# Kernel tuning notes

Hardware: AMD Instinct MI355X
Metric: run time of the kernel (lower is better)

## Reference

```python
import jax, jax.numpy as jnp
import numpy as np
from jax import lax

# Lens/aperture geometry (must match init_kwargs lens_mask)
LENS = 21
RADIUS = LENS // 2
EPS = 1e-8


def _offsets():
    """Flattened 21x21 aperture footprint: distance kernel, circular lens mask,
    and (row, col) slice offsets into the padded image."""
    ys, xs = np.meshgrid(np.arange(LENS), np.arange(LENS), indexing='ij')
    dy = ys - RADIUS
    dx = xs - RADIUS
    dist = np.sqrt(dy * dy + dx * dx).astype(np.float32)
    mask = (dist <= RADIUS).astype(np.float32)
    return (jnp.asarray(dist.ravel()), jnp.asarray(mask.ravel()),
            jnp.asarray(ys.ravel().astype(np.int32)),
            jnp.asarray(xs.ravel().astype(np.int32)))


def scatter_layer(x5, lens_effect):
    """Scatter (splat) defocus rendering of one RGBAD layer.

    x5: [B,5,H,W] (r,g,b,alpha,relative-disparity); lens_effect: [B,1].
    Each source pixel splats its premultiplied color over a disk of radius
    r = |disp| * lens_effect (soft-edged, area-normalized). Because the disk
    kernel is symmetric in the offset, the scatter is computed as a gather
    over the 21x21 footprint with weights taken from the *source* pixel.

    Returns [B,5,H,W]: [:3] accumulated rgb, [3] accumulated weight,
    [4] occupancy (clipped accumulated alpha-weight).
    """
    B, _, H, W = x5.shape
    dist, mask, oy, ox = _offsets()
    rgb, a, disp = x5[:, :3], x5[:, 3:4], x5[:, 4:5]
    r = jnp.clip(jnp.abs(disp) * lens_effect[:, :, None, None], 0.0, float(RADIUS))  # [B,1,H,W]

    # per-source-pixel soft disk area: sum_o mask(o) * clip(r + 0.5 - dist(o), 0, 1)
    def area_step(acc, dm):
        d, m = dm
        return acc + m * jnp.clip(r + 0.5 - d, 0.0, 1.0), None

    area, _ = lax.scan(area_step, jnp.zeros_like(r), (dist, mask))

    # premultiplied source energy, normalized by splat area
    s = jnp.concatenate([rgb * a, a], axis=1) / (area + EPS)  # [B,4,H,W]
    pad = ((0, 0), (0, 0), (RADIUS, RADIUS), (RADIUS, RADIUS))
    s_pad = jnp.pad(s, pad)
    r_pad = jnp.pad(r, pad)

    # gather formulation of the scatter: out[q] = sum_o s[q-o] * w(o; r[q-o])
    def step(acc, dmyx):
        d, m, dy, dx = dmyx
        sl = lax.dynamic_slice(s_pad, (0, 0, dy, dx), (B, 4, H, W))
        rsl = lax.dynamic_slice(r_pad, (0, 0, dy, dx), (B, 1, H, W))
        w = m * jnp.clip(rsl + 0.5 - d, 0.0, 1.0)
        return acc + sl * w, None

    out4, _ = lax.scan(step, jnp.zeros((B, 4, H, W), x5.dtype), (dist, mask, oy, ox))
    occu = jnp.clip(out4[:, 3:4], 0.0, 1.0)
    return jnp.concatenate([out4, occu], axis=1)


def setup_inputs() -> dict:
    key = jax.random.key(0)
    k1, k2 = jax.random.split(key)
    B, N_LAYER, H, W = 2, 3, 512, 512
    rgbad_layers = jax.random.uniform(k1, (B, 5 * N_LAYER, H, W), dtype=jnp.float32)
    # lens strength in a range that exercises the full 21x21 footprint
    lens_effect = jax.random.uniform(k2, (B, 1), dtype=jnp.float32) * 10.0
    focal = jnp.zeros((B, 5 * N_LAYER, H, W), dtype=jnp.float32)
    return {"rgbad_layers": rgbad_layers, "lens_effect": lens_effect, "focal": focal}


def reference(rgbad_layers, lens_effect, focal):
    """Multi_Layer_Renderer.forward: front-to-back alpha compositing of
    per-layer scatter-rendered bokeh."""
    x = rgbad_layers - focal
    n_layer = x.shape[1] // 5
    blurs = [scatter_layer(x[:, 5 * i:5 * (i + 1)], lens_effect) for i in range(n_layer)]
    rgb0, w0, o0 = blurs[0][:, :3], blurs[0][:, 3:4], blurs[0][:, 4:5]
    blur_rgb = rgb0 / (w0 + EPS) * o0
    trans = 1.0 - o0  # accumulated transmittance
    for li in range(1, n_layer):
        lr, lw, lo = blurs[li][:, :3], blurs[li][:, 3:4], blurs[li][:, 4:5]
        blur_rgb = blur_rgb + lr / (lw + EPS) * (trans * lo)
        trans = trans * (1.0 - lo)
    return blur_rgb
```

## Files before the change

kernel.cpp:

```cpp
#include <hip/hip_runtime.h>
#include <hip/hip_bf16.h>

#define HH 512
#define WW 512
#define HWSZ (512*512)

typedef _Float16 hh4 __attribute__((ext_vector_type(4)));
typedef _Float16 hh2 __attribute__((ext_vector_type(2)));
typedef float    ff4 __attribute__((ext_vector_type(4)));

__device__ __forceinline__ float clamp01(float x) {
    return __builtin_amdgcn_fmed3f(x, 0.0f, 1.0f);
}
__device__ __forceinline__ hh2 clamp01h2(hh2 x) {
    const hh2 z = {(_Float16)0.0f, (_Float16)0.0f};
    const hh2 o = {(_Float16)1.0f, (_Float16)1.0f};
    return __builtin_elementwise_min(__builtin_elementwise_max(x, z), o);
}
__device__ __forceinline__ hh2 pkrtz(float a, float b) {
    return __builtin_bit_cast(hh2, __builtin_amdgcn_cvt_pkrtz(a, b));
}

__global__ __launch_bounds__(256, 2)
void mlr_fused_kernel(const float* __restrict__ rgbad,
                      const float* __restrict__ lens_eff,
                      const float* __restrict__ focal,
                      float* __restrict__ out,
                      int nbx, int B)
{
    constexpr int TW = 64, TH = 16;
    constexpr int SW = 88;
    constexpr int SH = TH + 20;
    constexpr int LP = 90;
    constexpr int NG = SW / 4;
    constexpr int NSLOT = SH * NG;
    constexpr int NIT = (NSLOT + 255) / 256;

    __shared__ uint2 sP[SH * LP];
    __shared__ uint  rP[SH * LP / 2];
    __shared__ int   maxbits;

    const int tx  = threadIdx.x;
    const int ty  = threadIdx.y;
    const int tid = ty * 16 + tx;
    const int bid = blockIdx.x;
    const int bb  = bid % B;
    const int t   = bid / B;
    const int bx0 = (t % nbx) * TW;
    const int by0 = (t / nbx) * TH;
    const float lens = lens_eff[bb];

    static constexpr float DJ[44] = {
        0.f, 1.f, 1.41421356f, 2.f, 2.23606798f, 2.82842712f, 3.f, 3.16227766f,
        3.60555128f, 4.f, 4.12310563f, 4.24264069f, 4.47213595f, 5.f, 5.09901951f,
        5.38516481f, 5.65685425f, 5.83095189f, 6.f, 6.08276253f, 6.32455532f,
        6.40312424f, 6.70820393f, 7.f, 7.07106781f, 7.21110255f, 7.28010989f,
        7.61577311f, 7.81024968f, 8.f, 8.06225775f, 8.24621125f, 8.48528137f,
        8.54400375f, 8.60232527f, 8.94427191f, 9.f, 9.05538514f, 9.21954446f,
        9.43398113f, 9.48683298f, 9.84885780f, 9.89949494f, 10.f };
    static constexpr float CNT[44] = {
        1,4,4,4,8,4,4,8,8,4,8,4,8,12,8,8,4,8,4,8,8,8,
        8,4,12,8,8,8,8,4,16,8,4,8,8,8,4,8,16,8,8,8,4,12 };

    float blurR[4] = {0,0,0,0}, blurG[4] = {0,0,0,0}, blurB[4] = {0,0,0,0};
    float trans[4] = {1,1,1,1};

#pragma unroll 1
    for (int l = 0; l < 3; ++l) {
        __syncthreads();
        if (tid == 0) maxbits = 0;
        __syncthreads();

        const float* pin = rgbad + (size_t)(bb * 15 + 5 * l) * HWSZ;
        const float* pfo = focal + (size_t)(bb * 15 + 5 * l) * HWSZ;
        float mloc = 0.f;

#pragma unroll
        for (int it = 0; it < NIT; ++it) {
            int s = tid + it * 256;
            s = (s < NSLOT) ? s : (NSLOT - 1);
            const int row = s / NG;
            const int grp = s - row * NG;
            const int gy  = by0 - 10 + row;
            const int gx0 = bx0 - 12 + 4 * grp;

            ff4 i0 = {0,0,0,0}, i1 = {0,0,0,0}, i2 = {0,0,0,0}, i3 = {0,0,0,0}, i4 = {0,0,0,0};
            ff4 f0 = {0,0,0,0}, f1 = {0,0,0,0}, f2 = {0,0,0,0}, f3 = {0,0,0,0}, f4 = {0,0,0,0};
            const bool valid = ((unsigned)gy < (unsigned)HH) && ((unsigned)gx0 < (unsigned)WW);
            if (valid) {
                const size_t off = (size_t)gy * WW + (size_t)gx0;
                i0 = *reinterpret_cast<const ff4*>(pin + off);
                i1 = *reinterpret_cast<const ff4*>(pin + off +   HWSZ);
                i2 = *reinterpret_cast<const ff4*>(pin + off + 2*HWSZ);
                i3 = *reinterpret_cast<const ff4*>(pin + off + 3*HWSZ);
                i4 = *reinterpret_cast<const ff4*>(pin + off + 4*HWSZ);
                f0 = *reinterpret_cast<const ff4*>(pfo + off);
                f1 = *reinterpret_cast<const ff4*>(pfo + off +   HWSZ);
                f2 = *reinterpret_cast<const ff4*>(pfo + off + 2*HWSZ);
                f3 = *reinterpret_cast<const ff4*>(pfo + off + 3*HWSZ);
                f4 = *reinterpret_cast<const ff4*>(pfo + off + 4*HWSZ);
            }
            uint2 pk[4];
            unsigned short rh[4];
#pragma unroll
            for (int k = 0; k < 4; ++k) {
                const float cr = i0[k] - f0[k];
                const float cg = i1[k] - f1[k];
                const float cb = i2[k] - f2[k];
                const float ca = i3[k] - f3[k];
                const float cd = i4[k] - f4[k];
                const float r  = fminf(fabsf(cd) * lens, 10.f);
                const float rp05 = r + 0.5f;
                const hh2 rp2s = pkrtz(rp05, rp05);
                float aacc = 0.f;
#pragma unroll
                for (int j = 0; j < 44; j += 2) {
                    const hh2 dj2 = {(_Float16)DJ[j], (_Float16)DJ[j + 1]};
                    const hh2 c2  = {(_Float16)CNT[j], (_Float16)CNT[j + 1]};
                    const hh2 w2  = clamp01h2(rp2s - dj2);
                    aacc = __builtin_amdgcn_fdot2(w2, c2, aacc, false);
                }
                const float inv = 1.0f / (aacc + 1e-8f);
                const float pa  = ca * inv;
                hh4 hv;
                hv.x = (_Float16)(cr * pa);
                hv.y = (_Float16)(cg * pa);
                hv.z = (_Float16)(cb * pa);
                hv.w = (_Float16)pa;
                pk[k] = __builtin_bit_cast(uint2, hv);
                rh[k] = __builtin_bit_cast(unsigned short, (_Float16)rp05);
                mloc  = fmaxf(mloc, rp05);
            }
            const int base = row * LP + 4 * grp;
            uint4 s01, s23;
            s01.x = pk[0].x; s01.y = pk[0].y; s01.z = pk[1].x; s01.w = pk[1].y;
            s23.x = pk[2].x; s23.y = pk[2].y; s23.z = pk[3].x; s23.w = pk[3].y;
            *reinterpret_cast<uint4*>(&sP[base])     = s01;
            *reinterpret_cast<uint4*>(&sP[base + 2]) = s23;
            uint2 rr2;
            rr2.x = (uint)rh[0] | ((uint)rh[1] << 16);
            rr2.y = (uint)rh[2] | ((uint)rh[3] << 16);
            *reinterpret_cast<uint2*>(&rP[base >> 1]) = rr2;
        }
        atomicMax(&maxbits, __float_as_int(mloc));
        __syncthreads();

        const float rmax = __int_as_float(maxbits);
        const int U = min(10, (int)ceilf(rmax) - 1);

        float accR[4] = {0,0,0,0}, accG[4] = {0,0,0,0};
        float accB[4] = {0,0,0,0}, accW[4] = {0,0,0,0};

#define PAIRD(v0) { \
            const uint4 sp = *reinterpret_cast<const uint4*>(&sP[rbase + (v0)]); \
            const hh2 rp2 = __builtin_bit_cast(hh2, rP[(rbase + (v0)) >> 1]); \
            const hh2 cR = __builtin_bit_cast(hh2, __builtin_amdgcn_perm(sp.z, sp.x, 0x05040100u)); \
            const hh2 cG = __builtin_bit_cast(hh2, __builtin_amdgcn_perm(sp.z, sp.x, 0x07060302u)); \
            const hh2 cB = __builtin_bit_cast(hh2, __builtin_amdgcn_perm(sp.w, sp.y, 0x05040100u)); \
            const hh2 cA = __builtin_bit_cast(hh2, __builtin_amdgcn_perm(sp.w, sp.y, 0x07060302u)); \
            _Pragma("unroll") \
            for (int ox = 0; ox < 4; ++ox) { \
                const hh2 w2 = clamp01h2(rp2 - hdd2[(v0) - ox + 13]); \
                accR[ox] = __builtin_amdgcn_fdot2(cR, w2, accR[ox], false); \
                accG[ox] = __builtin_amdgcn_fdot2(cG, w2, accG[ox], false); \
                accB[ox] = __builtin_amdgcn_fdot2(cB, w2, accB[ox], false); \
                accW[ox] = __builtin_amdgcn_fdot2(cA, w2, accW[ox], false); \
            } }

#pragma unroll 1
        for (int u = -U; u <= U; ++u) {
            const float u2f = (float)(u * u);
            const float vm2 = rmax * rmax - u2f;
            hh2 hdd2[26];
#pragma unroll
            for (int m = 0; m < 26; ++m) {
                const int dxa = m - 13, dxb = dxa + 1;
                const float qa = u2f + (float)(dxa * dxa);
                const float qb = u2f + (float)(dxb * dxb);
                const float da = (qa <= 100.0f) ? __builtin_sqrtf(qa) : 3000.0f;
                const float db = (qb <= 100.0f) ? __builtin_sqrtf(qb) : 3000.0f;
                hdd2[m] = pkrtz(da, db);
            }
            const int rbase = (ty + 10 + u) * LP + 12 + 4 * tx;

            PAIRD(-2) PAIRD(0) PAIRD(2) PAIRD(4)
            if (vm2 > 9.0f)  { PAIRD(-6) PAIRD(-4) PAIRD(6) PAIRD(8) }
            if (vm2 > 36.0f) { PAIRD(-8) PAIRD(10) }
            if (vm2 > 81.0f) { PAIRD(-10) PAIRD(12) }
        }
#undef PAIRD

#pragma unroll
        for (int ox = 0; ox < 4; ++ox) {
            const float wsum = accW[ox];
            const float occ  = clamp01(wsum);
            const float f    = trans[ox] * occ / (wsum + 1e-8f);
            blurR[ox] = fmaf(accR[ox], f, blurR[ox]);
            blurG[ox] = fmaf(accG[ox], f, blurG[ox]);
            blurB[ox] = fmaf(accB[ox], f, blurB[ox]);
            trans[ox] *= (1.0f - occ);
        }
    }

    const int oy = by0 + ty;
    const size_t obase = (size_t)bb * 3 * HWSZ + (size_t)oy * WW + (size_t)(bx0 + 4 * tx);

    float4 vR, vG, vB;
    vR.x = blurR[0]; vR.y = blurR[1]; vR.z = blurR[2]; vR.w = blurR[3];
    vG.x = blurG[0]; vG.y = blurG[1]; vG.z = blurG[2]; vG.w = blurG[3];
    vB.x = blurB[0]; vB.y = blurB[1]; vB.z = blurB[2]; vB.w = blurB[3];

    *reinterpret_cast<float4*>(out + obase)            = vR;
    *reinterpret_cast<float4*>(out + obase + HWSZ)     = vG;
    *reinterpret_cast<float4*>(out + obase + 2 * HWSZ) = vB;
}

extern "C" void kernel_launch(void* const* d_in, const int* in_sizes, int n_in,
                              void* d_out, int out_size, void* d_ws, size_t ws_size,
                              hipStream_t stream) {
    const float* rgbad = (const float*)d_in[0];
    const float* lens  = (const float*)d_in[1];
    const float* focal = (const float*)d_in[2];
    float* out = (float*)d_out;
    const int B = in_sizes[1];
    const int nbx = WW / 64;
    const int nby = HH / 16;
    dim3 grid(nbx * nby * B, 1, 1);
    dim3 block(16, 16, 1);
    hipLaunchKernelGGL(mlr_fused_kernel, grid, block, 0, stream,
                       rgbad, lens, focal, out, nbx, B);
}
```

Before: 43.99 us.

## Compute two output rows per thread and share shared-memory loads across rows

Each thread now computes a 2-row by 4-column output block, using a 32x32 tile and a 128-thread block. Each loaded source row is used for two output rows at vertical offsets u and u-1, with the distance table from the previous iteration carried forward as the second row's table. This roughly halves LDS loads and distance-table builds per output. It costs more registers (doubled accumulators and two 26-entry tables), and the taller halo means more loaded pixels per output tile.

```diff
diff --git a/kernel.cpp b/kernel.cpp
--- a/kernel.cpp
+++ b/kernel.cpp
@@ -8,6 +8,14 @@
 typedef _Float16 hh4 __attribute__((ext_vector_type(4)));
 typedef _Float16 hh2 __attribute__((ext_vector_type(2)));
 typedef float    ff4 __attribute__((ext_vector_type(4)));
+
+constexpr int TW = 32, TH = 32;
+constexpr int SW = 56;
+constexpr int SH = 52;
+constexpr int LP = 60;
+constexpr int NG = SW / 4;
+constexpr int NSLOT = SH * NG;
+constexpr int NIT = 6;
 
 __device__ __forceinline__ float clamp01(float x) {
     return __builtin_amdgcn_fmed3f(x, 0.0f, 1.0f);
@@ -21,28 +29,20 @@
     return __builtin_bit_cast(hh2, __builtin_amdgcn_cvt_pkrtz(a, b));
 }
 
-__global__ __launch_bounds__(256, 2)
+__global__ __launch_bounds__(128, 2)
 void mlr_fused_kernel(const float* __restrict__ rgbad,
                       const float* __restrict__ lens_eff,
                       const float* __restrict__ focal,
                       float* __restrict__ out,
                       int nbx, int B)
 {
-    constexpr int TW = 64, TH = 16;
-    constexpr int SW = 88;
-    constexpr int SH = TH + 20;
-    constexpr int LP = 90;
-    constexpr int NG = SW / 4;
-    constexpr int NSLOT = SH * NG;
-    constexpr int NIT = (NSLOT + 255) / 256;
-
     __shared__ uint2 sP[SH * LP];
     __shared__ uint  rP[SH * LP / 2];
     __shared__ int   maxbits;
 
     const int tx  = threadIdx.x;
     const int ty  = threadIdx.y;
-    const int tid = ty * 16 + tx;
+    const int tid = ty * 8 + tx;
     const int bid = blockIdx.x;
     const int bb  = bid % B;
     const int t   = bid / B;
@@ -62,8 +62,10 @@
         1,4,4,4,8,4,4,8,8,4,8,4,8,12,8,8,4,8,4,8,8,8,
         8,4,12,8,8,8,8,4,16,8,4,8,8,8,4,8,16,8,8,8,4,12 };
 
-    float blurR[4] = {0,0,0,0}, blurG[4] = {0,0,0,0}, blurB[4] = {0,0,0,0};
-    float trans[4] = {1,1,1,1};
+    float blR[2][4] = {{0,0,0,0},{0,0,0,0}};
+    float blG[2][4] = {{0,0,0,0},{0,0,0,0}};
+    float blB[2][4] = {{0,0,0,0},{0,0,0,0}};
+    float trans[2][4] = {{1,1,1,1},{1,1,1,1}};
 
 #pragma unroll 1
     for (int l = 0; l < 3; ++l) {
@@ -77,7 +79,7 @@
 
 #pragma unroll
         for (int it = 0; it < NIT; ++it) {
-            int s = tid + it * 256;
+            int s = tid + it * 128;
             s = (s < NSLOT) ? s : (NSLOT - 1);
             const int row = s / NG;
             const int grp = s - row * NG;
@@ -147,72 +149,125 @@
 
         const float rmax = __int_as_float(maxbits);
         const int U = min(10, (int)ceilf(rmax) - 1);
-
-        float accR[4] = {0,0,0,0}, accG[4] = {0,0,0,0};
-        float accB[4] = {0,0,0,0}, accW[4] = {0,0,0,0};
-
-#define PAIRD(v0) { \
-            const uint4 sp = *reinterpret_cast<const uint4*>(&sP[rbase + (v0)]); \
-            const hh2 rp2 = __builtin_bit_cast(hh2, rP[(rbase + (v0)) >> 1]); \
-            const hh2 cR = __builtin_bit_cast(hh2, __builtin_amdgcn_perm(sp.z, sp.x, 0x05040100u)); \
-            const hh2 cG = __builtin_bit_cast(hh2, __builtin_amdgcn_perm(sp.z, sp.x, 0x07060302u)); \
-            const hh2 cB = __builtin_bit_cast(hh2, __builtin_amdgcn_perm(sp.w, sp.y, 0x05040100u)); \
-            const hh2 cA = __builtin_bit_cast(hh2, __builtin_amdgcn_perm(sp.w, sp.y, 0x07060302u)); \
+        const int auMax = min(11, U + 1);
+
+        float aR[2][4] = {{0,0,0,0},{0,0,0,0}};
+        float aG[2][4] = {{0,0,0,0},{0,0,0,0}};
+        float aB[2][4] = {{0,0,0,0},{0,0,0,0}};
+        float aW[2][4] = {{0,0,0,0},{0,0,0,0}};
+
+        hh2 T0[26], T1[26];
+#define BUILD_T(T_, U2F_) { \
+            _Pragma("unroll") \
+            for (int m = 0; m < 26; ++m) { \
+                const int dxa = m - 13, dxb = m - 12; \
+                const float qa = (U2F_) + (float)(dxa * dxa); \
+                const float qb = (U2F_) + (float)(dxb * dxb); \
+                const float da = (qa <= 100.0f) ? __builtin_sqrtf(qa) : 3000.0f; \
+                const float db = (qb <= 100.0f) ? __builtin_sqrtf(qb) : 3000.0f; \
+                T_[m] = pkrtz(da, db); \
+            } }
+
+        BUILD_T(T0, 0.0f)
+
+#define PCOMP2(SP_, RPH_, v0, TA_, TB_) { \
+            const hh2 rp2 = __builtin_bit_cast(hh2, (RPH_)); \
+            const hh2 cR = __builtin_bit_cast(hh2, __builtin_amdgcn_perm((SP_).z, (SP_).x, 0x05040100u)); \
+            const hh2 cG = __builtin_bit_cast(hh2, __builtin_amdgcn_perm((SP_).z, (SP_).x, 0x07060302u)); \
+            const hh2 cB = __builtin_bit_cast(hh2, __builtin_amdgcn_perm((SP_).w, (SP_).y, 0x05040100u)); \
+            const hh2 cA = __builtin_bit_cast(hh2, __builtin_amdgcn_perm((SP_).w, (SP_).y, 0x07060302u)); \
             _Pragma("unroll") \
             for (int ox = 0; ox < 4; ++ox) { \
-                const hh2 w2 = clamp01h2(rp2 - hdd2[(v0) - ox + 13]); \
-                accR[ox] = __builtin_amdgcn_fdot2(cR, w2, accR[ox], false); \
-                accG[ox] = __builtin_amdgcn_fdot2(cG, w2, accG[ox], false); \
-                accB[ox] = __builtin_amdgcn_fdot2(cB, w2, accB[ox], false); \
-                accW[ox] = __builtin_amdgcn_fdot2(cA, w2, accW[ox], false); \
+                const hh2 w0 = clamp01h2(rp2 - TA_[(v0) - ox + 13]); \
+                aR[0][ox] = __builtin_amdgcn_fdot2(cR, w0, aR[0][ox], false); \
+                aG[0][ox] = __builtin_amdgcn_fdot2(cG, w0, aG[0][ox], false); \
+                aB[0][ox] = __builtin_amdgcn_fdot2(cB, w0, aB[0][ox], false); \
+                aW[0][ox] = __builtin_amdgcn_fdot2(cA, w0, aW[0][ox], false); \
+                const hh2 w1 = clamp01h2(rp2 - TB_[(v0) - ox + 13]); \
+                aR[1][ox] = __builtin_amdgcn_fdot2(cR, w1, aR[1][ox], false); \
+                aG[1][ox] = __builtin_amdgcn_fdot2(cG, w1, aG[1][ox], false); \
+                aB[1][ox] = __builtin_amdgcn_fdot2(cB, w1, aB[1][ox], false); \
+                aW[1][ox] = __builtin_amdgcn_fdot2(cA, w1, aW[1][ox], false); \
             } }
+#define LDQ(nm, rb, off)   const uint2 nm = *reinterpret_cast<const uint2*>(&rP[((rb) + (off)) >> 1]);
+#define LD128(nm, rb, off) const uint4 nm = *reinterpret_cast<const uint4*>(&sP[(rb) + (off)]);
 
 #pragma unroll 1
-        for (int u = -U; u <= U; ++u) {
-            const float u2f = (float)(u * u);
-            const float vm2 = rmax * rmax - u2f;
-            hh2 hdd2[26];
-#pragma unroll
-            for (int m = 0; m < 26; ++m) {
-                const int dxa = m - 13, dxb = dxa + 1;
-                const float qa = u2f + (float)(dxa * dxa);
-                const float qb = u2f + (float)(dxb * dxb);
-                const float da = (qa <= 100.0f) ? __builtin_sqrtf(qa) : 3000.0f;
-                const float db = (qb <= 100.0f) ? __builtin_sqrtf(qb) : 3000.0f;
-                hdd2[m] = pkrtz(da, db);
-            }
-            const int rbase = (ty + 10 + u) * LP + 12 + 4 * tx;
-
-            PAIRD(-2) PAIRD(0) PAIRD(2) PAIRD(4)
-            if (vm2 > 9.0f)  { PAIRD(-6) PAIRD(-4) PAIRD(6) PAIRD(8) }
-            if (vm2 > 36.0f) { PAIRD(-8) PAIRD(10) }
-            if (vm2 > 81.0f) { PAIRD(-10) PAIRD(12) }
+        for (int au = 1; au <= auMax; ++au) {
+            const float au1 = (float)(au - 1);
+            const float vm2 = rmax * rmax - au1 * au1;
+            BUILD_T(T1, (float)(au * au))
+
+            const int rbA = (2 * ty + 10 + au)     * LP + 12 + 4 * tx;
+            const int rbB = (2 * ty + 10 + 1 - au) * LP + 12 + 4 * tx;
+
+            LDQ(qAm4, rbA, -4) LDQ(qA0, rbA, 0) LDQ(qA4, rbA, 4)
+            LD128(sAm2, rbA, -2) LD128(sA0, rbA, 0) LD128(sA2, rbA, 2) LD128(sA4, rbA, 4)
+            LDQ(qBm4, rbB, -4) LDQ(qB0, rbB, 0) LDQ(qB4, rbB, 4)
+            LD128(sBm2, rbB, -2) LD128(sB0, rbB, 0) LD128(sB2, rbB, 2) LD128(sB4, rbB, 4)
+            PCOMP2(sAm2, qAm4.y, -2, T1, T0) PCOMP2(sA0, qA0.x, 0, T1, T0)
+            PCOMP2(sA2,  qA0.y,  2, T1, T0) PCOMP2(sA4, qA4.x, 4, T1, T0)
+            PCOMP2(sBm2, qBm4.y, -2, T0, T1) PCOMP2(sB0, qB0.x, 0, T0, T1)
+            PCOMP2(sB2,  qB0.y,  2, T0, T1) PCOMP2(sB4, qB4.x, 4, T0, T1)
+            if (vm2 > 9.0f) {
+                LDQ(qAm8, rbA, -8) LDQ(qA8, rbA, 8)
+                LD128(sAm6, rbA, -6) LD128(sAm4, rbA, -4) LD128(sA6, rbA, 6) LD128(sA8, rbA, 8)
+                LDQ(qBm8, rbB, -8) LDQ(qB8, rbB, 8)
+                LD128(sBm6, rbB, -6) LD128(sBm4, rbB, -4) LD128(sB6, rbB, 6) LD128(sB8, rbB, 8)
+                PCOMP2(sAm6, qAm8.y, -6, T1, T0) PCOMP2(sAm4, qAm4.x, -4, T1, T0)
+                PCOMP2(sA6,  qA4.y,  6, T1, T0) PCOMP2(sA8,  qA8.x,  8, T1, T0)
+                PCOMP2(sBm6, qBm8.y, -6, T0, T1) PCOMP2(sBm4, qBm4.x, -4, T0, T1)
+                PCOMP2(sB6,  qB4.y,  6, T0, T1) PCOMP2(sB8,  qB8.x,  8, T0, T1)
+                if (vm2 > 36.0f) {
+                    LD128(sAm8, rbA, -8) LD128(sA10, rbA, 10)
+                    LD128(sBm8, rbB, -8) LD128(sB10, rbB, 10)
+                    PCOMP2(sAm8, qAm8.x, -8, T1, T0) PCOMP2(sA10, qA8.y, 10, T1, T0)
+                    PCOMP2(sBm8, qBm8.x, -8, T0, T1) PCOMP2(sB10, qB8.y, 10, T0, T1)
+                    if (vm2 > 81.0f) {
+                        LDQ(qAm12, rbA, -12) LDQ(qA12, rbA, 12)
+                        LD128(sAm10, rbA, -10) LD128(sA12, rbA, 12)
+                        LDQ(qBm12, rbB, -12) LDQ(qB12, rbB, 12)
+                        LD128(sBm10, rbB, -10) LD128(sB12, rbB, 12)
+                        PCOMP2(sAm10, qAm12.y, -10, T1, T0) PCOMP2(sA12, qA12.x, 12, T1, T0)
+                        PCOMP2(sBm10, qBm12.y, -10, T0, T1) PCOMP2(sB12, qB12.x, 12, T0, T1)
+                    }
+                }
+            }
+#pragma unroll
+            for (int m = 0; m < 26; ++m) T0[m] = T1[m];
         }
-#undef PAIRD
-
-#pragma unroll
-        for (int ox = 0; ox < 4; ++ox) {
-            const float wsum = accW[ox];
-            const float occ  = clamp01(wsum);
-            const float f    = trans[ox] * occ / (wsum + 1e-8f);
-            blurR[ox] = fmaf(accR[ox], f, blurR[ox]);
-            blurG[ox] = fmaf(accG[ox], f, blurG[ox]);
-            blurB[ox] = fmaf(accB[ox], f, blurB[ox]);
-            trans[ox] *= (1.0f - occ);
+#undef PCOMP2
+#undef LDQ
+#undef LD128
+#undef BUILD_T
+
+#pragma unroll
+        for (int rr = 0; rr < 2; ++rr) {
+#pragma unroll
+            for (int ox = 0; ox < 4; ++ox) {
+                const float wsum = aW[rr][ox];
+                const float occ  = clamp01(wsum);
+                const float f    = trans[rr][ox] * occ / (wsum + 1e-8f);
+                blR[rr][ox] = fmaf(aR[rr][ox], f, blR[rr][ox]);
+                blG[rr][ox] = fmaf(aG[rr][ox], f, blG[rr][ox]);
+                blB[rr][ox] = fmaf(aB[rr][ox], f, blB[rr][ox]);
+                trans[rr][ox] *= (1.0f - occ);
+            }
         }
     }
 
-    const int oy = by0 + ty;
-    const size_t obase = (size_t)bb * 3 * HWSZ + (size_t)oy * WW + (size_t)(bx0 + 4 * tx);
-
-    float4 vR, vG, vB;
-    vR.x = blurR[0]; vR.y = blurR[1]; vR.z = blurR[2]; vR.w = blurR[3];
-    vG.x = blurG[0]; vG.y = blurG[1]; vG.z = blurG[2]; vG.w = blurG[3];
-    vB.x = blurB[0]; vB.y = blurB[1]; vB.z = blurB[2]; vB.w = blurB[3];
-
-    *reinterpret_cast<float4*>(out + obase)            = vR;
-    *reinterpret_cast<float4*>(out + obase + HWSZ)     = vG;
-    *reinterpret_cast<float4*>(out + obase + 2 * HWSZ) = vB;
+#pragma unroll
+    for (int rr = 0; rr < 2; ++rr) {
+        const int oy = by0 + 2 * ty + rr;
+        const size_t obase = (size_t)bb * 3 * HWSZ + (size_t)oy * WW + (size_t)(bx0 + 4 * tx);
+        float4 vR, vG, vB;
+        vR.x = blR[rr][0]; vR.y = blR[rr][1]; vR.z = blR[rr][2]; vR.w = blR[rr][3];
+        vG.x = blG[rr][0]; vG.y = blG[rr][1]; vG.z = blG[rr][2]; vG.w = blG[rr][3];
+        vB.x = blB[rr][0]; vB.y = blB[rr][1]; vB.z = blB[rr][2]; vB.w = blB[rr][3];
+        *reinterpret_cast<float4*>(out + obase)            = vR;
+        *reinterpret_cast<float4*>(out + obase + HWSZ)     = vG;
+        *reinterpret_cast<float4*>(out + obase + 2 * HWSZ) = vB;
+    }
 }
 
 extern "C" void kernel_launch(void* const* d_in, const int* in_sizes, int n_in,
@@ -223,10 +278,10 @@
     const float* focal = (const float*)d_in[2];
     float* out = (float*)d_out;
     const int B = in_sizes[1];
-    const int nbx = WW / 64;
-    const int nby = HH / 16;
+    const int nbx = WW / TW;
+    const int nby = HH / TH;
     dim3 grid(nbx * nby * B, 1, 1);
-    dim3 block(16, 16, 1);
+    dim3 block(8, 16, 1);
     hipLaunchKernelGGL(mlr_fused_kernel, grid, block, 0, stream,
                        rgbad, lens, focal, out, nbx, B);
 }
```

New measurement: 60.58 us. 37.7% more time.

## Make row loop wave-uniform and batch radius loads into wider LDS reads

Applied to the files above, without the earlier changes.

The row loop now iterates over absolute staging rows shared by each group of 4 thread rows (one wavefront), so the trip count and band-width branches are uniform across the wave instead of diverging per thread. Each thread masks rows outside its own disk through the distance table, since entries beyond radius 10 are set to a large value. Radius values are fetched as 64-bit pairs and shared between neighbouring column offsets, which cuts LDS read instructions. The LDS row pitch goes from 90 to 92. In exchange, each thread processes up to 3 extra rows that contribute nothing, and the band width is chosen from the row nearest the centre within the wave.

```diff
diff --git a/kernel.cpp b/kernel.cpp
--- a/kernel.cpp
+++ b/kernel.cpp
@@ -8,6 +8,14 @@
 typedef _Float16 hh4 __attribute__((ext_vector_type(4)));
 typedef _Float16 hh2 __attribute__((ext_vector_type(2)));
 typedef float    ff4 __attribute__((ext_vector_type(4)));
+
+constexpr int TW = 64, TH = 16;
+constexpr int SW = 88;
+constexpr int SH = 36;
+constexpr int LP = 92;
+constexpr int NG = SW / 4;
+constexpr int NSLOT = SH * NG;
+constexpr int NIT = 4;
 
 __device__ __forceinline__ float clamp01(float x) {
     return __builtin_amdgcn_fmed3f(x, 0.0f, 1.0f);
@@ -28,14 +36,6 @@
                       float* __restrict__ out,
                       int nbx, int B)
 {
-    constexpr int TW = 64, TH = 16;
-    constexpr int SW = 88;
-    constexpr int SH = TH + 20;
-    constexpr int LP = 90;
-    constexpr int NG = SW / 4;
-    constexpr int NSLOT = SH * NG;
-    constexpr int NIT = (NSLOT + 255) / 256;
-
     __shared__ uint2 sP[SH * LP];
     __shared__ uint  rP[SH * LP / 2];
     __shared__ int   maxbits;
@@ -49,6 +49,7 @@
     const int bx0 = (t % nbx) * TW;
     const int by0 = (t / nbx) * TH;
     const float lens = lens_eff[bb];
+    const int wty0 = ty & ~3;
 
     static constexpr float DJ[44] = {
         0.f, 1.f, 1.41421356f, 2.f, 2.23606798f, 2.82842712f, 3.f, 3.16227766f,
@@ -151,26 +152,33 @@
         float accR[4] = {0,0,0,0}, accG[4] = {0,0,0,0};
         float accB[4] = {0,0,0,0}, accW[4] = {0,0,0,0};
 
-#define PAIRD(v0) { \
-            const uint4 sp = *reinterpret_cast<const uint4*>(&sP[rbase + (v0)]); \
-            const hh2 rp2 = __builtin_bit_cast(hh2, rP[(rbase + (v0)) >> 1]); \
-            const hh2 cR = __builtin_bit_cast(hh2, __builtin_amdgcn_perm(sp.z, sp.x, 0x05040100u)); \
-            const hh2 cG = __builtin_bit_cast(hh2, __builtin_amdgcn_perm(sp.z, sp.x, 0x07060302u)); \
-            const hh2 cB = __builtin_bit_cast(hh2, __builtin_amdgcn_perm(sp.w, sp.y, 0x05040100u)); \
-            const hh2 cA = __builtin_bit_cast(hh2, __builtin_amdgcn_perm(sp.w, sp.y, 0x07060302u)); \
-            _Pragma("unroll") \
-            for (int ox = 0; ox < 4; ++ox) { \
-                const hh2 w2 = clamp01h2(rp2 - hdd2[(v0) - ox + 13]); \
-                accR[ox] = __builtin_amdgcn_fdot2(cR, w2, accR[ox], false); \
-                accG[ox] = __builtin_amdgcn_fdot2(cG, w2, accG[ox], false); \
-                accB[ox] = __builtin_amdgcn_fdot2(cB, w2, accB[ox], false); \
-                accW[ox] = __builtin_amdgcn_fdot2(cA, w2, accW[ox], false); \
-            } }
-
+#define PCOMP(SP_, RPH_, v0) { \
+        const hh2 rp2 = __builtin_bit_cast(hh2, (RPH_)); \
+        const hh2 cR = __builtin_bit_cast(hh2, __builtin_amdgcn_perm((SP_).z, (SP_).x, 0x05040100u)); \
+        const hh2 cG = __builtin_bit_cast(hh2, __builtin_amdgcn_perm((SP_).z, (SP_).x, 0x07060302u)); \
+        const hh2 cB = __builtin_bit_cast(hh2, __builtin_amdgcn_perm((SP_).w, (SP_).y, 0x05040100u)); \
+        const hh2 cA = __builtin_bit_cast(hh2, __builtin_amdgcn_perm((SP_).w, (SP_).y, 0x07060302u)); \
+        _Pragma("unroll") \
+        for (int ox = 0; ox < 4; ++ox) { \
+            const hh2 w2 = clamp01h2(rp2 - hdd2[(v0) - ox + 13]); \
+            accR[ox] = __builtin_amdgcn_fdot2(cR, w2, accR[ox], false); \
+            accG[ox] = __builtin_amdgcn_fdot2(cG, w2, accG[ox], false); \
+            accB[ox] = __builtin_amdgcn_fdot2(cB, w2, accB[ox], false); \
+            accW[ox] = __builtin_amdgcn_fdot2(cA, w2, accW[ox], false); \
+        } }
+#define LDQ(nm, off)   const uint2 nm = *reinterpret_cast<const uint2*>(&rP[(rbase + (off)) >> 1]);
+#define LD128(nm, off) const uint4 nm = *reinterpret_cast<const uint4*>(&sP[rbase + (off)]);
+
+        const int R0 = wty0 + 10 - U;
+        const int R1 = wty0 + 13 + U;
 #pragma unroll 1
-        for (int u = -U; u <= U; ++u) {
+        for (int R = R0; R <= R1; ++R) {
+            const int u0   = R - 10 - wty0;
+            const int umin = max(0, max(u0 - 3, -u0));
+            const float vm2 = rmax * rmax - (float)(umin * umin);
+            const int u    = R - 10 - ty;
             const float u2f = (float)(u * u);
-            const float vm2 = rmax * rmax - u2f;
+
             hh2 hdd2[26];
 #pragma unroll
             for (int m = 0; m < 26; ++m) {
@@ -181,14 +189,32 @@
                 const float db = (qb <= 100.0f) ? __builtin_sqrtf(qb) : 3000.0f;
                 hdd2[m] = pkrtz(da, db);
             }
-            const int rbase = (ty + 10 + u) * LP + 12 + 4 * tx;
-
-            PAIRD(-2) PAIRD(0) PAIRD(2) PAIRD(4)
-            if (vm2 > 9.0f)  { PAIRD(-6) PAIRD(-4) PAIRD(6) PAIRD(8) }
-            if (vm2 > 36.0f) { PAIRD(-8) PAIRD(10) }
-            if (vm2 > 81.0f) { PAIRD(-10) PAIRD(12) }
+
+            const int rbase = R * LP + 12 + 4 * tx;
+
+            LDQ(q_m4, -4) LDQ(q_0, 0) LDQ(q_4, 4)
+            LD128(s_m2, -2) LD128(s_0, 0) LD128(s_2, 2) LD128(s_4, 4)
+            PCOMP(s_m2, q_m4.y, -2) PCOMP(s_0, q_0.x, 0)
+            PCOMP(s_2,  q_0.y,  2) PCOMP(s_4, q_4.x, 4)
+            if (vm2 > 9.0f) {
+                LDQ(q_m8, -8) LDQ(q_8, 8)
+                LD128(s_m6, -6) LD128(s_m4, -4) LD128(s_6, 6) LD128(s_8, 8)
+                PCOMP(s_m6, q_m8.y, -6) PCOMP(s_m4, q_m4.x, -4)
+                PCOMP(s_6,  q_4.y,  6) PCOMP(s_8,  q_8.x,  8)
+                if (vm2 > 36.0f) {
+                    LD128(s_m8, -8) LD128(s_10, 10)
+                    PCOMP(s_m8, q_m8.x, -8) PCOMP(s_10, q_8.y, 10)
+                    if (vm2 > 81.0f) {
+                        LDQ(q_m12, -12) LDQ(q_12, 12)
+                        LD128(s_m10, -10) LD128(s_12, 12)
+                        PCOMP(s_m10, q_m12.y, -10) PCOMP(s_12, q_12.x, 12)
+                    }
+                }
+            }
         }
-#undef PAIRD
+#undef PCOMP
+#undef LDQ
+#undef LD128
 
 #pragma unroll
         for (int ox = 0; ox < 4; ++ox) {
@@ -223,8 +249,8 @@
     const float* focal = (const float*)d_in[2];
     float* out = (float*)d_out;
     const int B = in_sizes[1];
-    const int nbx = WW / 64;
-    const int nby = HH / 16;
+    const int nbx = WW / TW;
+    const int nby = HH / TH;
     dim3 grid(nbx * nby * B, 1, 1);
     dim3 block(16, 16, 1);
     hipLaunchKernelGGL(mlr_fused_kernel, grid, block, 0, stream,
```

New measurement: 51.04 us. 16.0% more time.
